# Kernel optimization log

Hardware: AMD Instinct MI355X
Metric: run time of the kernel (lower is better)

Reference implementation:

```python
import jax, jax.numpy as jnp
import numpy as np

NUM_HEADS = 12
WIN = 7  # window_size[0] == window_size[1]


def setup_inputs() -> dict:
    key = jax.random.key(0)
    ks = jax.random.split(key, 8)
    B_, N, C = 2048, WIN * WIN, 384
    nW = 64
    return {
        "x": jax.random.normal(ks[0], (B_, N, C), dtype=jnp.float32),
        "mask": jax.random.normal(ks[1], (nW, N, N), dtype=jnp.float32),
        "qkv_w": jax.random.normal(ks[2], (3 * C, C), dtype=jnp.float32) * 0.02,
        "qkv_b": jax.random.normal(ks[3], (3 * C,), dtype=jnp.float32) * 0.02,
        "proj_w": jax.random.normal(ks[4], (C, C), dtype=jnp.float32) * 0.02,
        "proj_b": jax.random.normal(ks[5], (C,), dtype=jnp.float32) * 0.02,
        "rpb_table": jax.random.normal(ks[6], ((2 * WIN - 1) ** 2, NUM_HEADS), dtype=jnp.float32) * 0.02,
        "rel_index": jax.random.randint(ks[7], (N * N,), 0, (2 * WIN - 1) ** 2, dtype=jnp.int32),
    }


def reference(x, mask, qkv_w, qkv_b, proj_w, proj_b, rpb_table, rel_index):
    B_, N, C = x.shape
    H = NUM_HEADS
    d = C // H
    scale = d ** -0.5

    # QKV projection (quant wrappers act as identity in non-quant state)
    qkv = x @ qkv_w.T + qkv_b                      # [B_, N, 3C]
    qkv = qkv.reshape(B_, N, 3, H, d).transpose(2, 0, 3, 1, 4)  # [3, B_, H, N, d]
    q, k, v = qkv[0], qkv[1], qkv[2]

    attn = jnp.einsum("bhnd,bhmd->bhnm", q * scale, k)  # [B_, H, N, N]

    # relative position bias gather: [N*N] -> [N, N, H] -> [H, N, N]
    bias = rpb_table[rel_index].reshape(N, N, H).transpose(2, 0, 1)
    attn = attn + bias[None]

    # shifted-window mask add
    nW = mask.shape[0]
    attn = attn.reshape(B_ // nW, nW, H, N, N) + mask[None, :, None]
    attn = attn.reshape(B_, H, N, N)

    attn = jax.nn.softmax(attn, axis=-1)

    out = jnp.einsum("bhnm,bhmd->bhnd", attn, v)   # [B_, H, N, d]
    out = out.transpose(0, 2, 1, 3).reshape(B_, N, C)
    out = out @ proj_w.T + proj_b
    return out, attn
```

## Files before the change

kernel.cpp:

```cpp
#include <hip/hip_runtime.h>
#include <hip/hip_bf16.h>
#include <stdint.h>

#define H_ 12
#define D_ 32
#define N_ 49
#define C_ 384
#define B_TOT 2048
#define BH 24576
#define M_ROWS 100352
#define SCALE 0.17677669529663689f

typedef float f32x4 __attribute__((ext_vector_type(4)));
typedef __bf16 bf16x8 __attribute__((ext_vector_type(8)));
typedef unsigned short ushortx8 __attribute__((ext_vector_type(8)));

static __device__ __forceinline__ unsigned short f2bf(float f) {
  __bf16 b = (__bf16)f;
  return __builtin_bit_cast(unsigned short, b);
}

__global__ void cast_bf16(const float* __restrict__ in,
                          unsigned short* __restrict__ out, int n8) {
  int i = blockIdx.x * blockDim.x + threadIdx.x;
  const int stride = gridDim.x * blockDim.x;
  for (; i < n8; i += stride) {
    float4 a = ((const float4*)in)[2 * i];
    float4 b = ((const float4*)in)[2 * i + 1];
    ushortx8 v;
    v[0] = f2bf(a.x); v[1] = f2bf(a.y); v[2] = f2bf(a.z); v[3] = f2bf(a.w);
    v[4] = f2bf(b.x); v[5] = f2bf(b.y); v[6] = f2bf(b.z); v[7] = f2bf(b.w);
    *(ushortx8*)&out[(size_t)i * 8] = v;
  }
}

__global__ void build_comb(const float* __restrict__ mask,
                           const float* __restrict__ rpb,
                           const int* __restrict__ ridx,
                           float* __restrict__ comb) {
  const int h = blockIdx.x, w = blockIdx.y;
  float* cb = comb + (size_t)(w * H_ + h) * 4096;
  const float* mw = mask + (size_t)w * N_ * N_;
  for (int e = threadIdx.x; e < 4096; e += 256) {
    const int r = e >> 6, c = e & 63;
    float v;
    if (c >= N_) v = -1e30f;
    else if (r >= N_) v = 0.0f;
    else v = mw[r * N_ + c] + rpb[ridx[r * N_ + c] * H_ + h];
    cb[e] = v;
  }
}

__global__ __launch_bounds__(256, 3)
void qkv_gemm(const unsigned short* __restrict__ A,
              const unsigned short* __restrict__ W,
              const float* __restrict__ bias, unsigned short* __restrict__ qkv) {
  __shared__ __align__(16) unsigned short smem[20480];
  unsigned short* lA0 = smem;
  unsigned short* lB0 = smem + 10240;
  const int tid = threadIdx.x;
  const int w = blockIdx.x;
  const int t = (w & 7) * 882 + (w >> 3);
  const int bm = t / 9, bn = t - bm * 9;

  const int lane = tid & 63, wv = tid >> 6;
  const int wm = wv >> 1, wn = wv & 1;
  const int lo = lane & 15, hi = lane >> 4;
  const int r0 = tid >> 2, r1 = r0 + 64;
  const int off = (tid & 3) * 8;

  const unsigned short* Ab = A + (size_t)bm * 128 * 384;
  const unsigned short* Wb = W + (size_t)bn * 128 * 384;

  f32x4 acc[4][4];
#pragma unroll
  for (int i = 0; i < 4; i++)
#pragma unroll
    for (int j = 0; j < 4; j++)
#pragma unroll
      for (int r = 0; r < 4; r++) acc[i][j][r] = 0.0f;

  *(uint4*)&lA0[r0 * 40 + off] = *(const uint4*)(Ab + r0 * 384 + off);
  *(uint4*)&lA0[r1 * 40 + off] = *(const uint4*)(Ab + r1 * 384 + off);
  *(uint4*)&lB0[r0 * 40 + off] = *(const uint4*)(Wb + r0 * 384 + off);
  *(uint4*)&lB0[r1 * 40 + off] = *(const uint4*)(Wb + r1 * 384 + off);
  __syncthreads();

  int buf = 0;
  for (int kt = 0; kt < 12; kt++) {
    uint4 pa0, pa1, pb0, pb1;
    if (kt < 11) {
      const int kc = (kt + 1) * 32 + off;
      pa0 = *(const uint4*)(Ab + r0 * 384 + kc);
      pa1 = *(const uint4*)(Ab + r1 * 384 + kc);
      pb0 = *(const uint4*)(Wb + r0 * 384 + kc);
      pb1 = *(const uint4*)(Wb + r1 * 384 + kc);
    }
    const unsigned short* la = lA0 + buf * 5120;
    const unsigned short* lb = lB0 + buf * 5120;
    bf16x8 af[4], bfm[4];
#pragma unroll
    for (int mt = 0; mt < 4; mt++)
      af[mt] = *(const bf16x8*)&la[(wm * 64 + mt * 16 + lo) * 40 + hi * 8];
#pragma unroll
    for (int nt = 0; nt < 4; nt++)
      bfm[nt] = *(const bf16x8*)&lb[(wn * 64 + nt * 16 + lo) * 40 + hi * 8];
#pragma unroll
    for (int mt = 0; mt < 4; mt++)
#pragma unroll
      for (int nt = 0; nt < 4; nt++)
        acc[mt][nt] = __builtin_amdgcn_mfma_f32_16x16x32_bf16(af[mt], bfm[nt], acc[mt][nt], 0, 0, 0);
    if (kt < 11) {
      unsigned short* wa = lA0 + (buf ^ 1) * 5120;
      unsigned short* wb = lB0 + (buf ^ 1) * 5120;
      *(uint4*)&wa[r0 * 40 + off] = pa0;
      *(uint4*)&wa[r1 * 40 + off] = pa1;
      *(uint4*)&wb[r0 * 40 + off] = pb0;
      *(uint4*)&wb[r1 * 40 + off] = pb1;
    }
    __syncthreads();
    buf ^= 1;
  }

  unsigned short* ep = smem + wv * 5120;
#pragma unroll
  for (int nt = 0; nt < 4; nt++) {
    const int j = bn * 128 + wn * 64 + nt * 16 + lo;
    const float bj = bias[j];
    const float mul = (j < 384) ? SCALE : 1.0f;
    const int ch = nt >> 1;
    const int dd = (nt & 1) * 16 + lo;
#pragma unroll
    for (int mt = 0; mt < 4; mt++) {
#pragma unroll
      for (int r = 0; r < 4; r++) {
        const int row = mt * 16 + hi * 4 + r;
        ep[(row * 2 + ch) * 40 + dd] = f2bf((acc[mt][nt][r] + bj) * mul);
      }
    }
  }
#pragma unroll
  for (int cc = 0; cc < 2; cc++) {
    const int cidx = cc * 64 + lane;
    const int lr = cidx >> 1, lch = cidx & 1;
    const int i = bm * 128 + wm * 64 + lr;
    const int b = i / 49, sq = i - b * 49;
    const int j0 = bn * 128 + wn * 64 + lch * 32;
    const int which = j0 / 384;
    const int rem = j0 - which * 384;
    const int h = rem >> 5;
    unsigned short* dst = qkv + ((size_t)which * BH + (size_t)b * H_ + h) * (N_ * D_) + sq * D_;
    const unsigned short* src = ep + cidx * 40;
#pragma unroll
    for (int q = 0; q < 4; q++)
      *(uint4*)(dst + q * 8) = *(const uint4*)(src + q * 8);
  }
}

__global__ __launch_bounds__(384, 1)
void attn_proj(const unsigned short* __restrict__ qkv,
               const float* __restrict__ comb,
               const unsigned short* __restrict__ wp,
               const float* __restrict__ pbias,
               float* __restrict__ probs,
               float* __restrict__ out) {
  __shared__ __align__(16) unsigned short avl[64 * 384];
  __shared__ __align__(16) unsigned short Pw[6][64 * 72];
  __shared__ __align__(16) unsigned short VTw[6][32 * 72];
  const int tid = threadIdx.x;
  const int wv = tid / 64, lane = tid & 63;
  const int lo = lane & 15, hi = lane >> 4;
  const int b = blockIdx.x;

  unsigned short* P = Pw[wv];
  unsigned short* VT = VTw[wv];

  {
    unsigned int* vz = (unsigned int*)VT;
#pragma unroll
    for (int i = 0; i < 18; i++) vz[lane + 64 * i] = 0u;
  }

#pragma unroll
  for (int hh = 0; hh < 2; hh++) {
    const int h = wv * 2 + hh;
    const unsigned short* qp = qkv + (size_t)(b * H_ + h) * (N_ * D_);
    const unsigned short* kp = qp + (size_t)BH * (N_ * D_);
    const unsigned short* vp = kp + (size_t)BH * (N_ * D_);

    bf16x8 aq[4], bk[4];
#pragma unroll
    for (int t = 0; t < 4; t++) {
      aq[t] = *(const bf16x8*)(qp + (t * 16 + lo) * D_ + hi * 8);
      bk[t] = *(const bf16x8*)(kp + (t * 16 + lo) * D_ + hi * 8);
    }
    f32x4 s[4][4];
#pragma unroll
    for (int mt = 0; mt < 4; mt++)
#pragma unroll
      for (int nt = 0; nt < 4; nt++) {
#pragma unroll
        for (int r = 0; r < 4; r++) s[mt][nt][r] = 0.0f;
        s[mt][nt] = __builtin_amdgcn_mfma_f32_16x16x32_bf16(aq[mt], bk[nt], s[mt][nt], 0, 0, 0);
      }

#pragma unroll
    for (int it = 0; it < 4; it++) {
      const int idx = it * 64 + lane;
      if (idx < 196) {
        const int sq = idx >> 2, ch = idx & 3;
        ushortx8 vv = *(const ushortx8*)(vp + sq * D_ + ch * 8);
#pragma unroll
        for (int jj = 0; jj < 8; jj++) VT[(ch * 8 + jj) * 72 + sq] = vv[jj];
      }
    }

    const float* cb = comb + (size_t)((b & 63) * H_ + h) * 4096;
#pragma unroll
    for (int mt = 0; mt < 4; mt++) {
#pragma unroll
      for (int r = 0; r < 4; r++) {
        const int row = mt * 16 + hi * 4 + r;
        const float* crow = cb + row * 64 + lo;
        float v0 = s[mt][0][r] + crow[0];
        float v1 = s[mt][1][r] + crow[16];
        float v2 = s[mt][2][r] + crow[32];
        float v3 = s[mt][3][r] + crow[48];
        float m = fmaxf(fmaxf(v0, v1), fmaxf(v2, v3));
        m = fmaxf(m, __shfl_xor(m, 1));
        m = fmaxf(m, __shfl_xor(m, 2));
        m = fmaxf(m, __shfl_xor(m, 4));
        m = fmaxf(m, __shfl_xor(m, 8));
        v0 = __expf(v0 - m); v1 = __expf(v1 - m);
        v2 = __expf(v2 - m); v3 = __expf(v3 - m);
        float sum = v0 + v1 + v2 + v3;
        sum += __shfl_xor(sum, 1);
        sum += __shfl_xor(sum, 2);
        sum += __shfl_xor(sum, 4);
        sum += __shfl_xor(sum, 8);
        const float rinv = 1.0f / sum;
        s[mt][0][r] = v0 * rinv; s[mt][1][r] = v1 * rinv;
        s[mt][2][r] = v2 * rinv; s[mt][3][r] = v3 * rinv;
      }
    }

    const size_t pbase = (size_t)(b * H_ + h) * N_ * N_;
#pragma unroll
    for (int mt = 0; mt < 4; mt++) {
#pragma unroll
      for (int r = 0; r < 4; r++) {
        const int row = mt * 16 + hi * 4 + r;
        if (row < N_) {
#pragma unroll
          for (int nt = 0; nt < 4; nt++) {
            const int c = nt * 16 + lo;
            if (c < N_) probs[pbase + row * N_ + c] = s[mt][nt][r];
          }
        }
#pragma unroll
        for (int nt = 0; nt < 4; nt++)
          P[row * 72 + nt * 16 + lo] = f2bf(s[mt][nt][r]);
      }
    }

    f32x4 o[4][2];
#pragma unroll
    for (int mt = 0; mt < 4; mt++)
#pragma unroll
      for (int n2 = 0; n2 < 2; n2++)
#pragma unroll
        for (int r = 0; r < 4; r++) o[mt][n2][r] = 0.0f;
#pragma unroll
    for (int ks = 0; ks < 2; ks++) {
      bf16x8 pa[4], vb[2];
#pragma unroll
      for (int mt = 0; mt < 4; mt++)
        pa[mt] = *(const bf16x8*)&P[(mt * 16 + lo) * 72 + ks * 32 + hi * 8];
#pragma unroll
      for (int n2 = 0; n2 < 2; n2++)
        vb[n2] = *(const bf16x8*)&VT[(n2 * 16 + lo) * 72 + ks * 32 + hi * 8];
#pragma unroll
      for (int mt = 0; mt < 4; mt++)
#pragma unroll
        for (int n2 = 0; n2 < 2; n2++)
          o[mt][n2] = __builtin_amdgcn_mfma_f32_16x16x32_bf16(pa[mt], vb[n2], o[mt][n2], 0, 0, 0);
    }

#pragma unroll
    for (int mt = 0; mt < 4; mt++) {
#pragma unroll
      for (int r = 0; r < 4; r++) {
        const int row = mt * 16 + hi * 4 + r;
#pragma unroll
        for (int n2 = 0; n2 < 2; n2++) {
          const int col = h * 32 + n2 * 16 + lo;
          const int chn = ((col >> 3) ^ (row & 7));
          avl[row * 384 + chn * 8 + (col & 7)] = f2bf(o[mt][n2][r]);
        }
      }
    }
  }

  __syncthreads();

  const int jb = wv * 64;
  f32x4 acc[4][4];
#pragma unroll
  for (int i = 0; i < 4; i++)
#pragma unroll
    for (int j = 0; j < 4; j++)
#pragma unroll
      for (int r = 0; r < 4; r++) acc[i][j][r] = 0.0f;

  for (int kt = 0; kt < 12; kt++) {
    bf16x8 af[4], bf[4];
#pragma unroll
    for (int mt = 0; mt < 4; mt++) {
      const int row = mt * 16 + lo;
      const int chn = ((kt * 4 + hi) ^ (row & 7));
      af[mt] = *(const bf16x8*)&avl[row * 384 + chn * 8];
    }
#pragma unroll
    for (int nt = 0; nt < 4; nt++)
      bf[nt] = *(const bf16x8*)(wp + (size_t)(jb + nt * 16 + lo) * 384 + kt * 32 + hi * 8);
#pragma unroll
    for (int mt = 0; mt < 4; mt++)
#pragma unroll
      for (int nt = 0; nt < 4; nt++)
        acc[mt][nt] = __builtin_amdgcn_mfma_f32_16x16x32_bf16(af[mt], bf[nt], acc[mt][nt], 0, 0, 0);
  }

#pragma unroll
  for (int nt = 0; nt < 4; nt++) {
    const int j = jb + nt * 16 + lo;
    const float bj = pbias[j];
#pragma unroll
    for (int mt = 0; mt < 4; mt++) {
#pragma unroll
      for (int r = 0; r < 4; r++) {
        const int row = mt * 16 + hi * 4 + r;
        if (row < N_)
          out[((size_t)b * N_ + row) * C_ + j] = acc[mt][nt][r] + bj;
      }
    }
  }
}

extern "C" void kernel_launch(void* const* d_in, const int* in_sizes, int n_in,
                              void* d_out, int out_size, void* d_ws, size_t ws_size,
                              hipStream_t stream) {
  const float* x      = (const float*)d_in[0];
  const float* mask   = (const float*)d_in[1];
  const float* qkv_w  = (const float*)d_in[2];
  const float* qkv_b  = (const float*)d_in[3];
  const float* proj_w = (const float*)d_in[4];
  const float* proj_b = (const float*)d_in[5];
  const float* rpb    = (const float*)d_in[6];
  const int*   ridx   = (const int*)d_in[7];

  unsigned short* qkv   = (unsigned short*)d_ws;
  unsigned short* x_bf  = qkv + (size_t)3 * BH * N_ * D_;
  float* comb           = (float*)(x_bf + (size_t)M_ROWS * C_);
  unsigned short* wq_bf = (unsigned short*)(comb + 768 * 4096);
  unsigned short* wp_bf = wq_bf + 1152 * 384;
  float* out   = (float*)d_out;
  float* probs = out + (size_t)M_ROWS * C_;

  cast_bf16<<<2048, 256, 0, stream>>>(x, x_bf, M_ROWS * C_ / 8);
  cast_bf16<<<216, 256, 0, stream>>>(qkv_w, wq_bf, 1152 * 384 / 8);
  cast_bf16<<<72, 256, 0, stream>>>(proj_w, wp_bf, 384 * 384 / 8);
  build_comb<<<dim3(H_, 64), 256, 0, stream>>>(mask, rpb, ridx, comb);
  qkv_gemm<<<7056, 256, 0, stream>>>(x_bf, wq_bf, qkv_b, qkv);
  attn_proj<<<2048, 384, 0, stream>>>(qkv, comb, wp_bf, proj_b, probs, out);
}
```

Before: 486.8 us.

## Drop LDS staging for V and attention output to raise attn_proj occupancy

The attn_proj kernel no longer stages transposed V and the per-block attention output in shared memory. V fragments are loaded directly from global memory with strided scalar loads, and the attention output is written to a global scratch buffer (reusing the x_bf region) and read back for the projection GEMM. Launch bounds now allow 3 blocks per CU. The goal is more concurrent blocks, paid for with extra global/L2 traffic, uncoalesced V loads, and reads of padding rows that now come from neighbouring data instead of zeros.

```diff
diff --git a/kernel.cpp b/kernel.cpp
--- a/kernel.cpp
+++ b/kernel.cpp
@@ -157,29 +157,20 @@
   }
 }
 
-__global__ __launch_bounds__(384, 1)
+__global__ __launch_bounds__(384, 3)
 void attn_proj(const unsigned short* __restrict__ qkv,
                const float* __restrict__ comb,
                const unsigned short* __restrict__ wp,
                const float* __restrict__ pbias,
                float* __restrict__ probs,
+               unsigned short* __restrict__ avg,
                float* __restrict__ out) {
-  __shared__ __align__(16) unsigned short avl[64 * 384];
   __shared__ __align__(16) unsigned short Pw[6][64 * 72];
-  __shared__ __align__(16) unsigned short VTw[6][32 * 72];
   const int tid = threadIdx.x;
   const int wv = tid / 64, lane = tid & 63;
   const int lo = lane & 15, hi = lane >> 4;
   const int b = blockIdx.x;
-
   unsigned short* P = Pw[wv];
-  unsigned short* VT = VTw[wv];
-
-  {
-    unsigned int* vz = (unsigned int*)VT;
-#pragma unroll
-    for (int i = 0; i < 18; i++) vz[lane + 64 * i] = 0u;
-  }
 
 #pragma unroll
   for (int hh = 0; hh < 2; hh++) {
@@ -203,17 +194,6 @@
         for (int r = 0; r < 4; r++) s[mt][nt][r] = 0.0f;
         s[mt][nt] = __builtin_amdgcn_mfma_f32_16x16x32_bf16(aq[mt], bk[nt], s[mt][nt], 0, 0, 0);
       }
-
-#pragma unroll
-    for (int it = 0; it < 4; it++) {
-      const int idx = it * 64 + lane;
-      if (idx < 196) {
-        const int sq = idx >> 2, ch = idx & 3;
-        ushortx8 vv = *(const ushortx8*)(vp + sq * D_ + ch * 8);
-#pragma unroll
-        for (int jj = 0; jj < 8; jj++) VT[(ch * 8 + jj) * 72 + sq] = vv[jj];
-      }
-    }
 
     const float* cb = comb + (size_t)((b & 63) * H_ + h) * 4096;
 #pragma unroll
@@ -277,8 +257,12 @@
       for (int mt = 0; mt < 4; mt++)
         pa[mt] = *(const bf16x8*)&P[(mt * 16 + lo) * 72 + ks * 32 + hi * 8];
 #pragma unroll
-      for (int n2 = 0; n2 < 2; n2++)
-        vb[n2] = *(const bf16x8*)&VT[(n2 * 16 + lo) * 72 + ks * 32 + hi * 8];
+      for (int n2 = 0; n2 < 2; n2++) {
+        const unsigned short* vcol = vp + n2 * 16 + lo;
+#pragma unroll
+        for (int j = 0; j < 8; j++)
+          vb[n2][j] = __builtin_bit_cast(__bf16, vcol[(ks * 32 + hi * 8 + j) * D_]);
+      }
 #pragma unroll
       for (int mt = 0; mt < 4; mt++)
 #pragma unroll
@@ -291,11 +275,10 @@
 #pragma unroll
       for (int r = 0; r < 4; r++) {
         const int row = mt * 16 + hi * 4 + r;
-#pragma unroll
-        for (int n2 = 0; n2 < 2; n2++) {
-          const int col = h * 32 + n2 * 16 + lo;
-          const int chn = ((col >> 3) ^ (row & 7));
-          avl[row * 384 + chn * 8 + (col & 7)] = f2bf(o[mt][n2][r]);
+        if (row < N_) {
+#pragma unroll
+          for (int n2 = 0; n2 < 2; n2++)
+            avg[((size_t)b * N_ + row) * C_ + h * D_ + n2 * 16 + lo] = f2bf(o[mt][n2][r]);
         }
       }
     }
@@ -304,6 +287,7 @@
   __syncthreads();
 
   const int jb = wv * 64;
+  const unsigned short* arow = avg + (size_t)b * N_ * C_;
   f32x4 acc[4][4];
 #pragma unroll
   for (int i = 0; i < 4; i++)
@@ -315,11 +299,8 @@
   for (int kt = 0; kt < 12; kt++) {
     bf16x8 af[4], bf[4];
 #pragma unroll
-    for (int mt = 0; mt < 4; mt++) {
-      const int row = mt * 16 + lo;
-      const int chn = ((kt * 4 + hi) ^ (row & 7));
-      af[mt] = *(const bf16x8*)&avl[row * 384 + chn * 8];
-    }
+    for (int mt = 0; mt < 4; mt++)
+      af[mt] = *(const bf16x8*)(arow + (size_t)(mt * 16 + lo) * C_ + kt * 32 + hi * 8);
 #pragma unroll
     for (int nt = 0; nt < 4; nt++)
       bf[nt] = *(const bf16x8*)(wp + (size_t)(jb + nt * 16 + lo) * 384 + kt * 32 + hi * 8);
@@ -360,6 +341,7 @@
 
   unsigned short* qkv   = (unsigned short*)d_ws;
   unsigned short* x_bf  = qkv + (size_t)3 * BH * N_ * D_;
+  unsigned short* avg   = x_bf;
   float* comb           = (float*)(x_bf + (size_t)M_ROWS * C_);
   unsigned short* wq_bf = (unsigned short*)(comb + 768 * 4096);
   unsigned short* wp_bf = wq_bf + 1152 * 384;
@@ -371,5 +353,5 @@
   cast_bf16<<<72, 256, 0, stream>>>(proj_w, wp_bf, 384 * 384 / 8);
   build_comb<<<dim3(H_, 64), 256, 0, stream>>>(mask, rpb, ridx, comb);
   qkv_gemm<<<7056, 256, 0, stream>>>(x_bf, wq_bf, qkv_b, qkv);
-  attn_proj<<<2048, 384, 0, stream>>>(qkv, comb, wp_bf, proj_b, probs, out);
-}
+  attn_proj<<<2048, 384, 0, stream>>>(qkv, comb, wp_bf, proj_b, probs, avg, out);
+}
```

New measurement: 623.0 us. 1.28x slower.

## Alias attention scratch with output tile in LDS to allow more resident blocks

Applied to the files above, without the earlier changes.

Shared memory drops from separate avl/P/VT arrays to one 72KB buffer: the per-wave P and V^T tiles are laid out with row stride 64 and an XOR swizzle instead of padding, and the attention output is held in packed registers until after a barrier, then written into the same region as avl. Launch bounds are raised to 3 blocks per CU so more blocks can be resident. This is meant to hide latency better through occupancy, at the cost of an extra barrier, more live registers, and a tighter register budget that could cause spills.

```diff
diff --git a/kernel.cpp b/kernel.cpp
--- a/kernel.cpp
+++ b/kernel.cpp
@@ -157,29 +157,30 @@
   }
 }
 
-__global__ __launch_bounds__(384, 1)
+__global__ __launch_bounds__(384, 3)
 void attn_proj(const unsigned short* __restrict__ qkv,
                const float* __restrict__ comb,
                const unsigned short* __restrict__ wp,
                const float* __restrict__ pbias,
                float* __restrict__ probs,
                float* __restrict__ out) {
-  __shared__ __align__(16) unsigned short avl[64 * 384];
-  __shared__ __align__(16) unsigned short Pw[6][64 * 72];
-  __shared__ __align__(16) unsigned short VTw[6][32 * 72];
+  __shared__ __align__(16) unsigned short smem[36864];
   const int tid = threadIdx.x;
   const int wv = tid / 64, lane = tid & 63;
   const int lo = lane & 15, hi = lane >> 4;
   const int b = blockIdx.x;
-
-  unsigned short* P = Pw[wv];
-  unsigned short* VT = VTw[wv];
+  unsigned short* P  = smem + wv * 4096;
+  unsigned short* VT = smem + 24576 + wv * 2048;
+  unsigned short* avl = smem;
+  const int l7 = lo & 7;
 
   {
     unsigned int* vz = (unsigned int*)VT;
 #pragma unroll
-    for (int i = 0; i < 18; i++) vz[lane + 64 * i] = 0u;
-  }
+    for (int i = 0; i < 16; i++) vz[lane + 64 * i] = 0u;
+  }
+
+  uint32_t opk[2][4][2][2];
 
 #pragma unroll
   for (int hh = 0; hh < 2; hh++) {
@@ -211,7 +212,8 @@
         const int sq = idx >> 2, ch = idx & 3;
         ushortx8 vv = *(const ushortx8*)(vp + sq * D_ + ch * 8);
 #pragma unroll
-        for (int jj = 0; jj < 8; jj++) VT[(ch * 8 + jj) * 72 + sq] = vv[jj];
+        for (int jj = 0; jj < 8; jj++)
+          VT[(ch * 8 + jj) * 64 + (((sq >> 3) ^ jj) << 3) + (sq & 7)] = vv[jj];
       }
     }
 
@@ -257,9 +259,10 @@
             if (c < N_) probs[pbase + row * N_ + c] = s[mt][nt][r];
           }
         }
+        const int r7 = row & 7;
 #pragma unroll
         for (int nt = 0; nt < 4; nt++)
-          P[row * 72 + nt * 16 + lo] = f2bf(s[mt][nt][r]);
+          P[row * 64 + (((nt * 2 + (lo >> 3)) ^ r7) << 3) + l7] = f2bf(s[mt][nt][r]);
       }
     }
 
@@ -275,10 +278,10 @@
       bf16x8 pa[4], vb[2];
 #pragma unroll
       for (int mt = 0; mt < 4; mt++)
-        pa[mt] = *(const bf16x8*)&P[(mt * 16 + lo) * 72 + ks * 32 + hi * 8];
+        pa[mt] = *(const bf16x8*)&P[(mt * 16 + lo) * 64 + (((ks * 4 + hi) ^ l7) << 3)];
 #pragma unroll
       for (int n2 = 0; n2 < 2; n2++)
-        vb[n2] = *(const bf16x8*)&VT[(n2 * 16 + lo) * 72 + ks * 32 + hi * 8];
+        vb[n2] = *(const bf16x8*)&VT[(n2 * 16 + lo) * 64 + (((ks * 4 + hi) ^ l7) << 3)];
 #pragma unroll
       for (int mt = 0; mt < 4; mt++)
 #pragma unroll
@@ -287,15 +290,31 @@
     }
 
 #pragma unroll
-    for (int mt = 0; mt < 4; mt++) {
-#pragma unroll
-      for (int r = 0; r < 4; r++) {
-        const int row = mt * 16 + hi * 4 + r;
-#pragma unroll
-        for (int n2 = 0; n2 < 2; n2++) {
-          const int col = h * 32 + n2 * 16 + lo;
-          const int chn = ((col >> 3) ^ (row & 7));
-          avl[row * 384 + chn * 8 + (col & 7)] = f2bf(o[mt][n2][r]);
+    for (int mt = 0; mt < 4; mt++)
+#pragma unroll
+      for (int n2 = 0; n2 < 2; n2++)
+#pragma unroll
+        for (int p = 0; p < 2; p++)
+          opk[hh][mt][n2][p] = (uint32_t)f2bf(o[mt][n2][2 * p]) |
+                               ((uint32_t)f2bf(o[mt][n2][2 * p + 1]) << 16);
+  }
+
+  __syncthreads();
+
+#pragma unroll
+  for (int hh = 0; hh < 2; hh++) {
+    const int col0 = (wv * 2 + hh) * 32;
+#pragma unroll
+    for (int mt = 0; mt < 4; mt++) {
+#pragma unroll
+      for (int n2 = 0; n2 < 2; n2++) {
+        const int col = col0 + n2 * 16 + lo;
+#pragma unroll
+        for (int r = 0; r < 4; r++) {
+          const int row = mt * 16 + hi * 4 + r;
+          const unsigned short v =
+              (unsigned short)(opk[hh][mt][n2][r >> 1] >> ((r & 1) * 16));
+          avl[row * 384 + (((col >> 3) ^ (row & 7)) << 3) + (col & 7)] = v;
         }
       }
     }
```

After: 700.6 us. 43.9% more time.
